# Kernel optimization log

Measured on AMD Instinct MI355X. Metric: run time of the kernel, lower is better.

Reference implementation:

```python
import jax, jax.numpy as jnp
import numpy as np

B, C, H, W = 4, 64, 64, 64
CQ = C // 2

def setup_inputs() -> dict:
    key = jax.random.key(0)
    ks = jax.random.split(key, 7)
    return {
        "x":  jax.random.normal(ks[0], (B, C, H, W), dtype=jnp.float32),
        "Wq": jax.random.normal(ks[1], (CQ, C), dtype=jnp.float32) * 0.05,
        "bq": jax.random.normal(ks[2], (CQ,), dtype=jnp.float32) * 0.05,
        "Wk": jax.random.normal(ks[3], (CQ, C), dtype=jnp.float32) * 0.05,
        "bk": jax.random.normal(ks[4], (CQ,), dtype=jnp.float32) * 0.05,
        "Wl": jax.random.normal(ks[5], (C, C), dtype=jnp.float32) * 0.05,
        "bl": jax.random.normal(ks[6], (C,), dtype=jnp.float32) * 0.05,
    }

def reference(x, Wq, bq, Wk, bk, Wl, bl):
    b, c, h, w = x.shape
    hw = h * w
    xf = x.reshape(b, c, hw)                                   # [B,C,HW]
    # 1x1 convs == per-pixel linear projections
    q = jnp.einsum('oc,bci->boi', Wq, xf) + bq[None, :, None]  # [B,CQ,HW]
    k = jnp.einsum('oc,bci->boi', Wk, xf) + bk[None, :, None]  # [B,CQ,HW]
    # energy[b,i,j] = <q[:,i], k[:,j]>  (proj_query permuted to [B,HW,CQ])
    energy = jnp.einsum('bci,bcj->bij', q, k)                  # [B,HW,HW]
    attn = jax.nn.softmax(energy, axis=-1)                     # softmax over last dim (keys j)
    # torch.bmm(proj_value, attention): out[b,c,j] = sum_i value[b,c,i] * attn[b,i,j]
    out = jnp.einsum('bci,bij->bcj', xf, attn)                 # [B,C,HW]
    out = out.reshape(b, c, h, w)
    out = jnp.einsum('oc,bchw->bohw', Wl, out) + bl[None, :, None, None]
    return out + x
```

## Files before the change

kernel.cpp:

```cpp
#include <hip/hip_runtime.h>
#include <hip/hip_bf16.h>


#define HW 4096
#define BN 4
#define CD 64
#define ISPL 8
#define LOG2E 1.44269504f

typedef short bf16x8 __attribute__((ext_vector_type(8)));
typedef float f32x4 __attribute__((ext_vector_type(4)));

static __device__ inline unsigned bfbits(float f) {
    union { float f; unsigned u; } v{f};
    return (v.u + 0x8000u) >> 16;
}
static __device__ inline float b2f(short s) {
    unsigned u = ((unsigned)(unsigned short)s) << 16;
    float f; __builtin_memcpy(&f, &u, 4); return f;
}
static __device__ inline int cvtpk(float lo, float hi) {
    __hip_bfloat162 h = __float22bfloat162_rn(make_float2(lo, hi));
    int r; __builtin_memcpy(&r, &h, 4); return r;
}
static __device__ inline void gl16(const void* g, void* l) {
    __builtin_amdgcn_global_load_lds(
        (const __attribute__((address_space(1))) unsigned int*)g,
        (__attribute__((address_space(3))) unsigned int*)l, 16, 0, 0);
}



__global__ __launch_bounds__(256, 4) void k_proj(
    const float* __restrict__ x, const float* __restrict__ Wq, const float* __restrict__ bq,
    const float* __restrict__ Wk, const float* __restrict__ bk, const float* __restrict__ Wl,
    short* __restrict__ Qt, short* __restrict__ Kt, short* __restrict__ Yc)
{
    __shared__ __align__(16) char sm[18944];
    short* WcL   = (short*)sm;
    short* xT    = (short*)(sm + 16384);
    float* biasL = (float*)(sm + 18432);

    int t = threadIdx.x;
    int wv = t >> 6, l = t & 63, g = l >> 4, n = l & 15;

    {
        int row = t >> 1, half = t & 1;
        const float* src; float scale = 1.f;
        if (row < 32)      { src = Wq + row * CD; scale = LOG2E; }
        else if (row < 64) { src = Wk + (row - 32) * CD; }
        else               { src = Wl + (row - 64) * CD; }
        int pk[16];
#pragma unroll
        for (int e = 0; e < 16; ++e)
            pk[e] = cvtpk(src[half * 32 + 2 * e] * scale, src[half * 32 + 2 * e + 1] * scale);
#pragma unroll
        for (int q = 0; q < 4; ++q)
            *(int4*)(WcL + row * 64 + ((((half << 2) + q) ^ (row & 7)) << 3)) =
                make_int4(pk[4 * q], pk[4 * q + 1], pk[4 * q + 2], pk[4 * q + 3]);
        if (half == 0)
            biasL[row] = (row < 32) ? LOG2E * bq[row] : (row < 64) ? bk[row - 32] : 0.f;
    }
    int pix0 = blockIdx.x << 4;
    {
        int c = t >> 2, q = t & 3;
        int b = pix0 >> 12, pxb = pix0 & (HW - 1);
        float4 v = *(const float4*)(x + ((size_t)b << 18) + ((size_t)c << 12) + pxb + q * 4);
        float vv[4] = {v.x, v.y, v.z, v.w};
#pragma unroll
        for (int e = 0; e < 4; ++e) {
            int px = q * 4 + e;
            xT[px * 64 + (((c >> 3) ^ (px & 7)) << 3) + (c & 7)] = (short)bfbits(vv[e]);
        }
    }
    __syncthreads();

    bf16x8 B0 = *(const bf16x8*)(xT + n * 64 + ((g ^ (n & 7)) << 3));
    bf16x8 B1 = *(const bf16x8*)(xT + n * 64 + (((4 + g) ^ (n & 7)) << 3));
    int pg = pix0 + n;
#pragma unroll
    for (int mm = 0; mm < 2; ++mm) {
        int mt = wv * 2 + mm;
        bf16x8 A0 = *(const bf16x8*)(WcL + (mt * 16 + n) * 64 + ((g ^ (n & 7)) << 3));
        bf16x8 A1 = *(const bf16x8*)(WcL + (mt * 16 + n) * 64 + (((4 + g) ^ (n & 7)) << 3));
        f32x4 d = {0.f, 0.f, 0.f, 0.f};
        d = __builtin_amdgcn_mfma_f32_16x16x32_bf16(A0, B0, d, 0, 0, 0);
        d = __builtin_amdgcn_mfma_f32_16x16x32_bf16(A1, B1, d, 0, 0, 0);
        d += *(const f32x4*)(biasL + mt * 16 + g * 4);
        if (mt < 4) {
            short* dst = (mt < 2 ? Qt : Kt) + ((size_t)pg << 5) + ((mt & 1) << 4) + (g << 2);
            *(int2*)dst = make_int2(cvtpk(d[0], d[1]), cvtpk(d[2], d[3]));
        } else {
            int ch2 = (mt - 4) * 16 + g * 4;
            int bb = pg >> 12, ii = pg & (HW - 1);
#pragma unroll
            for (int r = 0; r < 4; ++r)
                Yc[(((size_t)(bb * CD + ch2 + r)) << 12) + ii] = (short)bfbits(d[r]);
        }
    }
}


__global__ __launch_bounds__(256, 4) void k_pass1m(
    const short* __restrict__ Qt, const short* __restrict__ Kt, float* __restrict__ Spart)
{
    __shared__ float red[256];
    int t = threadIdx.x;
    int wv = t >> 6, l = t & 63, g = l >> 4, n = l & 15;
    int ch = blockIdx.x;
    int b = ch & 3, jq = (ch >> 2) & 3, i0 = (ch >> 4) << 6;
    size_t bHW = (size_t)b << 12;

    bf16x8 aq[4];
#pragma unroll
    for (int it = 0; it < 4; ++it)
        aq[it] = *(const bf16x8*)(Qt + ((bHW + i0 + it * 16 + n) << 5) + (g << 3));

    f32x4 ls[4];
#pragma unroll
    for (int it = 0; it < 4; ++it) ls[it] = (f32x4){0.f, 0.f, 0.f, 0.f};

    const short* kbase = Kt + ((bHW + jq * 1024 + wv * 256 + n) << 5) + (g << 3);
#pragma unroll 4
    for (int jt = 0; jt < 16; ++jt) {
        bf16x8 bkv = *(const bf16x8*)(kbase + jt * 512);
#pragma unroll
        for (int it = 0; it < 4; ++it) {
            f32x4 z = {0.f, 0.f, 0.f, 0.f};
            f32x4 s = __builtin_amdgcn_mfma_f32_16x16x32_bf16(aq[it], bkv, z, 0, 0, 0);
            ls[it][0] += exp2f(s[0]); ls[it][1] += exp2f(s[1]);
            ls[it][2] += exp2f(s[2]); ls[it][3] += exp2f(s[3]);
        }
    }
#pragma unroll
    for (int msk = 1; msk < 16; msk <<= 1)
#pragma unroll
        for (int it = 0; it < 4; ++it) {
            ls[it][0] += __shfl_xor(ls[it][0], msk, 64);
            ls[it][1] += __shfl_xor(ls[it][1], msk, 64);
            ls[it][2] += __shfl_xor(ls[it][2], msk, 64);
            ls[it][3] += __shfl_xor(ls[it][3], msk, 64);
        }
    if (n == 0)
#pragma unroll
        for (int it = 0; it < 4; ++it)
#pragma unroll
            for (int r = 0; r < 4; ++r)
                red[wv * 64 + it * 16 + g * 4 + r] = ls[it][r];
    __syncthreads();
    if (t < 64) {
        float s = red[t] + red[64 + t] + red[128 + t] + red[192 + t];
        Spart[(size_t)jq * 16384 + bHW + i0 + t] = s;
    }
}


__global__ __launch_bounds__(256, 4) void k_pass2(
    const short* __restrict__ Qt, const short* __restrict__ Kt,
    const short* __restrict__ Yc, const float* __restrict__ Spart,
    int* __restrict__ Opart)
{
    __shared__ __align__(16) char smem[36864];
    short* QtL = (short*)smem;
    short* W2L = (short*)(smem + 8192);
    short* Pb  = (short*)(smem + 24576);
    float* MtA = (float*)(smem + 34816);

    int t = threadIdx.x;
    int wv = t >> 6, l = t & 63, g = l >> 4, n = l & 15;
    int ch = blockIdx.x;
    int b = ch >> 8, isp = (ch >> 5) & 7, jt = ch & 31;
    int j0 = jt * 128 + wv * 32;
    size_t bHW = (size_t)b << 12;
    short* Pw = Pb + wv * 1280;

    bf16x8 bk0 = *(const bf16x8*)(Kt + ((bHW + j0 + n) << 5) + (g << 3));
    bf16x8 bk1 = *(const bf16x8*)(Kt + ((bHW + j0 + 16 + n) << 5) + (g << 3));

    f32x4 oacc[2][4];
#pragma unroll
    for (int a = 0; a < 2; ++a)
#pragma unroll
        for (int m = 0; m < 4; ++m) oacc[a][m] = (f32x4){0.f, 0.f, 0.f, 0.f};

    int swz = ((t & 7) ^ ((t >> 3) & 7)) << 4;
    const char* qsrc = (const char*)Qt + ((bHW + (size_t)isp * 512) << 6) + t * 16;
    const char* wsrc = (const char*)Yc + (((size_t)(b * CD + (t >> 3)) << 12) + isp * 512) * 2 + swz;
    char* qd0 = (char*)QtL + t * 16;  char* qd1 = qd0 + 4096;
    char* wd0 = (char*)W2L + t * 16;  char* wd1 = wd0 + 8192;

    gl16(qsrc, qd0);
    gl16(wsrc, wd0);
    gl16(wsrc + (32ull << 13), wd0 + 4096);
    if (t < 128) {
        const float* sp = Spart + bHW + (size_t)isp * 512 + t * 4;
        float4 a0 = *(const float4*)(sp);
        float4 a1 = *(const float4*)(sp + 16384);
        float4 a2 = *(const float4*)(sp + 32768);
        float4 a3 = *(const float4*)(sp + 49152);
        float4 mm;
        mm.x = -log2f(a0.x + a1.x + a2.x + a3.x);
        mm.y = -log2f(a0.y + a1.y + a2.y + a3.y);
        mm.z = -log2f(a0.z + a1.z + a2.z + a3.z);
        mm.w = -log2f(a0.w + a1.w + a2.w + a3.w);
        *(float4*)(MtA + t * 4) = mm;
    }
    asm volatile("s_waitcnt vmcnt(0) lgkmcnt(0)" ::: "memory");
    __builtin_amdgcn_s_barrier();
    __builtin_amdgcn_sched_barrier(0);

    const int NT = 8;
    for (int st = 0; st < NT; ++st) {
        int cur = st & 1;
        if (st > 0) {
            __builtin_amdgcn_s_barrier();
            __builtin_amdgcn_sched_barrier(0);
        }
        if (st + 1 < NT) {
            gl16(qsrc + (size_t)(st + 1) * 4096, cur ? qd0 : qd1);
            gl16(wsrc + (size_t)(st + 1) * 128, cur ? wd0 : wd1);
            gl16(wsrc + (size_t)(st + 1) * 128 + (32ull << 13), (cur ? wd0 : wd1) + 4096);
            asm volatile("s_waitcnt vmcnt(3)" ::: "memory");
        } else {
            asm volatile("s_waitcnt vmcnt(0)" ::: "memory");
        }
        __builtin_amdgcn_sched_barrier(0);

        const short* qL = QtL + cur * 2048;
        const char* wL = (const char*)W2L + cur * 8192;
        const float* mL = MtA + st * 64;
#pragma unroll
        for (int ks = 0; ks < 2; ++ks) {
            bf16x8 aq0 = *(const bf16x8*)(qL + (ks * 32 + n) * 32 + g * 8);
            bf16x8 aq1 = *(const bf16x8*)(qL + (ks * 32 + 16 + n) * 32 + g * 8);
            f32x4 cm0 = *(const f32x4*)(mL + ks * 32 + g * 4);
            f32x4 cm1 = *(const f32x4*)(mL + ks * 32 + 16 + g * 4);
            __builtin_amdgcn_s_setprio(1);
            f32x4 s00 = __builtin_amdgcn_mfma_f32_16x16x32_bf16(aq0, bk0, cm0, 0, 0, 0);
            f32x4 s01 = __builtin_amdgcn_mfma_f32_16x16x32_bf16(aq1, bk0, cm1, 0, 0, 0);
            f32x4 s10 = __builtin_amdgcn_mfma_f32_16x16x32_bf16(aq0, bk1, cm0, 0, 0, 0);
            f32x4 s11 = __builtin_amdgcn_mfma_f32_16x16x32_bf16(aq1, bk1, cm1, 0, 0, 0);
            __builtin_amdgcn_s_setprio(0);
            *(int2*)(Pw + n * 40 + 4 * g) =
                make_int2(cvtpk(exp2f(s00[0]), exp2f(s00[1])), cvtpk(exp2f(s00[2]), exp2f(s00[3])));
            *(int2*)(Pw + n * 40 + 16 + 4 * g) =
                make_int2(cvtpk(exp2f(s01[0]), exp2f(s01[1])), cvtpk(exp2f(s01[2]), exp2f(s01[3])));
            *(int2*)(Pw + (16 + n) * 40 + 4 * g) =
                make_int2(cvtpk(exp2f(s10[0]), exp2f(s10[1])), cvtpk(exp2f(s10[2]), exp2f(s10[3])));
            *(int2*)(Pw + (16 + n) * 40 + 16 + 4 * g) =
                make_int2(cvtpk(exp2f(s11[0]), exp2f(s11[1])), cvtpk(exp2f(s11[2]), exp2f(s11[3])));
            bf16x8 pb0 = *(const bf16x8*)(Pw + n * 40 + 8 * g);
            bf16x8 pb1 = *(const bf16x8*)(Pw + (16 + n) * 40 + 8 * g);
            __builtin_amdgcn_s_setprio(1);
#pragma unroll
            for (int mb = 0; mb < 4; ++mb) {
                bf16x8 aw = *(const bf16x8*)(wL + (mb * 16 + n) * 128 + ((((ks << 2) + g) ^ (n & 7)) << 4));
                oacc[0][mb] = __builtin_amdgcn_mfma_f32_16x16x32_bf16(aw, pb0, oacc[0][mb], 0, 0, 0);
                oacc[1][mb] = __builtin_amdgcn_mfma_f32_16x16x32_bf16(aw, pb1, oacc[1][mb], 0, 0, 0);
            }
            __builtin_amdgcn_s_setprio(0);
        }
        __builtin_amdgcn_sched_barrier(0);
    }
    size_t obase = ((size_t)(isp * BN + b)) << 17;
    int doff = jt * 64 + wv * 16 + n;
#pragma unroll
    for (int mb = 0; mb < 4; ++mb)
#pragma unroll
        for (int r = 0; r < 4; ++r) {
            int c = mb * 16 + g * 4 + r;
            Opart[obase + ((size_t)c << 11) + doff] =
                (int)bfbits(oacc[0][mb][r]) | ((int)bfbits(oacc[1][mb][r]) << 16);
        }
}


__global__ __launch_bounds__(256, 4) void k_merge(
    const int* __restrict__ Opart, const float* __restrict__ x,
    const float* __restrict__ bl, float* __restrict__ out)
{
    int T = blockIdx.x * 256 + threadIdx.x;
    int row = T >> 9;
    int u = T & 511;
    int g32 = u >> 2, sub = u & 3;
    int jlo = g32 * 32 + sub * 4;
    size_t rbase = (size_t)row << 12;
    float4 rl = *(const float4*)(x + rbase + jlo);
    float4 rh = *(const float4*)(x + rbase + jlo + 16);
    float bc = bl[row & 63];
    rl.x += bc; rl.y += bc; rl.z += bc; rl.w += bc;
    rh.x += bc; rh.y += bc; rh.z += bc; rh.w += bc;
    size_t dbase = ((size_t)row << 11) + g32 * 16 + sub * 4;
#pragma unroll
    for (int p = 0; p < ISPL; ++p) {
        int4 d = *(const int4*)(Opart + ((size_t)p << 19) + dbase);
        rl.x += b2f((short)(d.x & 0xffff)); rh.x += b2f((short)(d.x >> 16));
        rl.y += b2f((short)(d.y & 0xffff)); rh.y += b2f((short)(d.y >> 16));
        rl.z += b2f((short)(d.z & 0xffff)); rh.z += b2f((short)(d.z >> 16));
        rl.w += b2f((short)(d.w & 0xffff)); rh.w += b2f((short)(d.w >> 16));
    }
    *(float4*)(out + rbase + jlo) = rl;
    *(float4*)(out + rbase + jlo + 16) = rh;
}

extern "C" void kernel_launch(void* const* d_in, const int* in_sizes, int n_in,
                              void* d_out, int out_size, void* d_ws, size_t ws_size,
                              hipStream_t stream)
{
    (void)in_sizes; (void)n_in; (void)out_size; (void)ws_size;
    const float* x  = (const float*)d_in[0];
    const float* Wq = (const float*)d_in[1];
    const float* bq = (const float*)d_in[2];
    const float* Wk = (const float*)d_in[3];
    const float* bk = (const float*)d_in[4];
    const float* Wl = (const float*)d_in[5];
    const float* bl = (const float*)d_in[6];
    float* out = (float*)d_out;
    char* base = (char*)d_ws;

    short* Qt    = (short*)(base);
    short* Kt    = (short*)(base + 0x100000);
    short* Yc    = (short*)(base + 0x200000);
    float* Spart = (float*)(base + 0x500000);
    int*   Opart = (int*)(base + 0x540000);

    hipLaunchKernelGGL(k_proj, dim3(1024), dim3(256), 0, stream,
                       x, Wq, bq, Wk, bk, Wl, Qt, Kt, Yc);
    hipLaunchKernelGGL(k_pass1m, dim3(1024), dim3(256), 0, stream, Qt, Kt, Spart);
    hipLaunchKernelGGL(k_pass2, dim3(1024), dim3(256), 0, stream,
                       Qt, Kt, Yc, Spart, Opart);
    hipLaunchKernelGGL(k_merge, dim3(512), dim3(256), 0, stream, Opart, x, bl, out);
}
```

Before: 62.22 us.

## Fuse split-reduction merge into pass2 via last-arriving-block atomic counter

Removes the separate merge kernel launch. Each pass2 block increments a per-(batch, j-tile) counter after writing its partial output. The block that arrives last (count 7) sums all eight bf16 partials, adds bias and the residual, and writes the final output. The counters are zeroed in the projection kernel. This saves one launch and its tail, at the cost of threadfences, an atomic per block, and a serial merge done by the last block of each tile.

```diff
diff --git a/kernel.cpp b/kernel.cpp
--- a/kernel.cpp
+++ b/kernel.cpp
@@ -34,7 +34,8 @@
 __global__ __launch_bounds__(256, 4) void k_proj(
     const float* __restrict__ x, const float* __restrict__ Wq, const float* __restrict__ bq,
     const float* __restrict__ Wk, const float* __restrict__ bk, const float* __restrict__ Wl,
-    short* __restrict__ Qt, short* __restrict__ Kt, short* __restrict__ Yc)
+    short* __restrict__ Qt, short* __restrict__ Kt, short* __restrict__ Yc,
+    int* __restrict__ cnt)
 {
     __shared__ __align__(16) char sm[18944];
     short* WcL   = (short*)sm;
@@ -43,6 +44,8 @@
 
     int t = threadIdx.x;
     int wv = t >> 6, l = t & 63, g = l >> 4, n = l & 15;
+
+    if (blockIdx.x < 128 && t == 0) cnt[blockIdx.x] = 0;
 
     {
         int row = t >> 1, half = t & 1;
@@ -158,13 +161,16 @@
 __global__ __launch_bounds__(256, 4) void k_pass2(
     const short* __restrict__ Qt, const short* __restrict__ Kt,
     const short* __restrict__ Yc, const float* __restrict__ Spart,
-    int* __restrict__ Opart)
+    int* __restrict__ Opart, const float* __restrict__ x,
+    const float* __restrict__ bl, float* __restrict__ out,
+    int* __restrict__ cnt)
 {
     __shared__ __align__(16) char smem[36864];
     short* QtL = (short*)smem;
     short* W2L = (short*)(smem + 8192);
     short* Pb  = (short*)(smem + 24576);
     float* MtA = (float*)(smem + 34816);
+    __shared__ int s_tk;
 
     int t = threadIdx.x;
     int wv = t >> 6, l = t & 63, g = l >> 4, n = l & 15;
@@ -272,35 +278,37 @@
             Opart[obase + ((size_t)c << 11) + doff] =
                 (int)bfbits(oacc[0][mb][r]) | ((int)bfbits(oacc[1][mb][r]) << 16);
         }
-}
-
-
-__global__ __launch_bounds__(256, 4) void k_merge(
-    const int* __restrict__ Opart, const float* __restrict__ x,
-    const float* __restrict__ bl, float* __restrict__ out)
-{
-    int T = blockIdx.x * 256 + threadIdx.x;
-    int row = T >> 9;
-    int u = T & 511;
-    int g32 = u >> 2, sub = u & 3;
-    int jlo = g32 * 32 + sub * 4;
-    size_t rbase = (size_t)row << 12;
-    float4 rl = *(const float4*)(x + rbase + jlo);
-    float4 rh = *(const float4*)(x + rbase + jlo + 16);
-    float bc = bl[row & 63];
-    rl.x += bc; rl.y += bc; rl.z += bc; rl.w += bc;
-    rh.x += bc; rh.y += bc; rh.z += bc; rh.w += bc;
-    size_t dbase = ((size_t)row << 11) + g32 * 16 + sub * 4;
-#pragma unroll
-    for (int p = 0; p < ISPL; ++p) {
-        int4 d = *(const int4*)(Opart + ((size_t)p << 19) + dbase);
-        rl.x += b2f((short)(d.x & 0xffff)); rh.x += b2f((short)(d.x >> 16));
-        rl.y += b2f((short)(d.y & 0xffff)); rh.y += b2f((short)(d.y >> 16));
-        rl.z += b2f((short)(d.z & 0xffff)); rh.z += b2f((short)(d.z >> 16));
-        rl.w += b2f((short)(d.w & 0xffff)); rh.w += b2f((short)(d.w >> 16));
-    }
-    *(float4*)(out + rbase + jlo) = rl;
-    *(float4*)(out + rbase + jlo + 16) = rh;
+
+    __threadfence();
+    __syncthreads();
+    if (t == 0) s_tk = atomicAdd(&cnt[b * 32 + jt], 1);
+    __syncthreads();
+    if (s_tk == 7) {
+        __threadfence();
+        int c = t >> 2;
+        int jgrp = jt * 4 + (t & 3);
+        float bc = bl[c];
+        const int* Ob = Opart + ((size_t)b << 17) + ((size_t)c << 11) + (size_t)jgrp * 16;
+        const float* xr = x + (((size_t)(b * CD + c)) << 12) + jgrp * 32;
+        float* orow = out + (((size_t)(b * CD + c)) << 12) + jgrp * 32;
+#pragma unroll
+        for (int u = 0; u < 4; ++u) {
+            float4 rl = *(const float4*)(xr + u * 4);
+            float4 rh = *(const float4*)(xr + u * 4 + 16);
+            rl.x += bc; rl.y += bc; rl.z += bc; rl.w += bc;
+            rh.x += bc; rh.y += bc; rh.z += bc; rh.w += bc;
+#pragma unroll
+            for (int p = 0; p < ISPL; ++p) {
+                int4 d = *(const int4*)(Ob + ((size_t)p << 19) + u * 4);
+                rl.x += b2f((short)(d.x & 0xffff)); rh.x += b2f((short)(d.x >> 16));
+                rl.y += b2f((short)(d.y & 0xffff)); rh.y += b2f((short)(d.y >> 16));
+                rl.z += b2f((short)(d.z & 0xffff)); rh.z += b2f((short)(d.z >> 16));
+                rl.w += b2f((short)(d.w & 0xffff)); rh.w += b2f((short)(d.w >> 16));
+            }
+            *(float4*)(orow + u * 4) = rl;
+            *(float4*)(orow + u * 4 + 16) = rh;
+        }
+    }
 }
 
 extern "C" void kernel_launch(void* const* d_in, const int* in_sizes, int n_in,
@@ -323,11 +331,11 @@
     short* Yc    = (short*)(base + 0x200000);
     float* Spart = (float*)(base + 0x500000);
     int*   Opart = (int*)(base + 0x540000);
+    int*   cnt   = (int*)(base + 0x1540000);
 
     hipLaunchKernelGGL(k_proj, dim3(1024), dim3(256), 0, stream,
-                       x, Wq, bq, Wk, bk, Wl, Qt, Kt, Yc);
+                       x, Wq, bq, Wk, bk, Wl, Qt, Kt, Yc, cnt);
     hipLaunchKernelGGL(k_pass1m, dim3(1024), dim3(256), 0, stream, Qt, Kt, Spart);
     hipLaunchKernelGGL(k_pass2, dim3(1024), dim3(256), 0, stream,
-                       Qt, Kt, Yc, Spart, Opart);
-    hipLaunchKernelGGL(k_merge, dim3(512), dim3(256), 0, stream, Opart, x, bl, out);
-}
+                       Qt, Kt, Yc, Spart, Opart, x, bl, out, cnt);
+}
```

New measurement: 202.0 us. 225% more time.
